# Performance work log

Measured on AMD Instinct MI355X. Metric: run time of the kernel, lower is better.

## Reference

```python
import jax, jax.numpy as jnp
import numpy as np

B, P, D, N, K = 8, 784, 1536, 20000, 9


def setup_inputs() -> dict:
    key = jax.random.key(0)
    k1, k2 = jax.random.split(key)
    x = jax.random.normal(k1, (B, P, D), dtype=jnp.float32)       # patch embeddings [B, P, D]
    memory = jax.random.normal(k2, (N, D), dtype=jnp.float32)     # FAISS memory bank [N, D]
    return {"x": x, "memory": memory, "k": K}


def reference(x, memory, k):
    # Squared L2 distances (FAISS IndexFlatL2 convention): [B, P, N]
    x2 = jnp.sum(x * x, axis=-1, keepdims=True)                   # [B, P, 1]
    m2 = jnp.sum(memory * memory, axis=-1)                        # [N]
    d = x2 + m2[None, None, :] - 2.0 * jnp.einsum('bpd,nd->bpn', x, memory)
    # k nearest (smallest distances, ascending) -> score_patches [B, P, k]
    neg_topk, _ = jax.lax.top_k(-d, k)
    score_patches = -neg_topk
    closest_dist = score_patches[..., 0]                          # [B, P]
    idxmax = jnp.argmax(closest_dist, axis=1)                     # [B]
    # N_b: the k neighbor distances of the worst (max closest-dist) patch
    N_b = jnp.take_along_axis(score_patches, idxmax[:, None, None], axis=1)[:, 0, :]  # [B, k]
    N_b = N_b - jnp.max(N_b, axis=1, keepdims=True)               # numerical stabilization (as in source)
    N_b_exp = jnp.exp(N_b)
    w = 1.0 - jnp.max(N_b_exp, axis=1) / jnp.sum(N_b_exp, axis=1)  # [B]
    score = w * jnp.max(closest_dist, axis=1)                      # [B]
    return score
```

## Files before the change

### kernel.cpp

```cpp
#include <hip/hip_runtime.h>
#include <math.h>

#define B_    8
#define P_    784
#define M_    6272
#define D_    1536
#define N_    20000
#define NC_   4

#define MPAD  6400
#define NPAD2 20224
#define MT2   25
#define NT2   79
#define KT2   24

#define NBLK  625

using bf16x8 = __attribute__((ext_vector_type(8))) __bf16;
using f32x4v = __attribute__((ext_vector_type(4))) float;

#define GLD_LDS16(src, dst)                                            \
  __builtin_amdgcn_global_load_lds(                                    \
      (__attribute__((address_space(1))) const void*)(src),            \
      (__attribute__((address_space(3))) void*)(dst), 16, 0, 0)

__device__ __forceinline__ unsigned short f2bf(float f) {
  union { float f; unsigned u; } v; v.f = f;
  unsigned r = v.u + 0x7fffu + ((v.u >> 16) & 1u);
  return (unsigned short)(r >> 16);
}

__device__ __forceinline__ unsigned fenc(float f) {
  unsigned u = __float_as_uint(f);
  return (u >> 31) ? ~u : (u | 0x80000000u);
}
__device__ __forceinline__ float fdec(unsigned k) {
  return (k >> 31) ? __uint_as_float(k & 0x7FFFFFFFu) : __uint_as_float(~k);
}

__device__ __forceinline__ void convert_one(const float* __restrict__ src,
                                            unsigned short* __restrict__ dst,
                                            float* __restrict__ sq,
                                            int row, int realrows) {
  const int t = threadIdx.x;
  if (row >= realrows) {
    ushort4* w4 = (ushort4*)(dst + (size_t)row * D_);
    for (int i = t; i < D_ / 4; i += 256) w4[i] = ushort4{0, 0, 0, 0};
    if (t == 0) sq[row] = 1e30f;
    return;
  }
  const float4* r4 = (const float4*)(src + (size_t)row * D_);
  ushort4* w4 = (ushort4*)(dst + (size_t)row * D_);
  float s = 0.f;
  for (int i = t; i < D_ / 4; i += 256) {
    float4 v = r4[i];
    s += v.x * v.x + v.y * v.y + v.z * v.z + v.w * v.w;
    w4[i] = ushort4{f2bf(v.x), f2bf(v.y), f2bf(v.z), f2bf(v.w)};
  }
#pragma unroll
  for (int m = 32; m >= 1; m >>= 1) s += __shfl_xor(s, m);
  __shared__ float ws4[4];
  if ((t & 63) == 0) ws4[t >> 6] = s;
  __syncthreads();
  if (t == 0) sq[row] = ws4[0] + ws4[1] + ws4[2] + ws4[3];
}

__global__ void convert_all(const float* __restrict__ x, const float* __restrict__ mem,
                            unsigned short* __restrict__ xbf, unsigned short* __restrict__ mbf,
                            float* __restrict__ x2, float* __restrict__ m2) {
  const int blk = blockIdx.x;
  if (blk < NPAD2) convert_one(mem, mbf, m2, blk, N_);
  else convert_one(x, xbf, x2, blk - NPAD2, M_);
}

__global__ __launch_bounds__(512, 2) void gemm_min8(
    const unsigned short* __restrict__ xbf, const unsigned short* __restrict__ mbf,
    const float* __restrict__ m2, unsigned* __restrict__ closest_enc) {
  __shared__ __attribute__((aligned(16))) char ldsFlat[131072];
  __shared__ float ldsMin[4][256];

  const int NWG = MT2 * NT2;
  const int bid = blockIdx.x;
  const int q = NWG >> 3, r = NWG & 7;
  const int xcd = bid & 7, loc = bid >> 3;
  const int wg = (xcd < r ? xcd * (q + 1) : r * (q + 1) + (xcd - r) * q) + loc;
  const int s = wg / (5 * NT2);
  const int r2 = wg - s * (5 * NT2);
  const int mT = s * 5 + (r2 % 5);
  const int nT = r2 / 5;

  const int tid = threadIdx.x;
  const int lane = tid & 63, wid = tid >> 6;
  const int wm = wid >> 2, wn = wid & 3;
  const int g = lane >> 4, r16 = lane & 15;
  const int mBase = mT * 256, nBase = nT * 256;

  const int stRow = wid * 8 + (lane >> 3);
  const int stA = mBase + stRow;
  const int stB = nBase + stRow;
  const int cswz8 = ((lane & 7) ^ ((lane >> 3) & 7)) * 8;

  const int cs0 = (g * 16) ^ ((r16 & 7) << 4);
  const int rdA = wm * 16384 + r16 * 128;
  const int rdB = wn * 8192 + r16 * 128;

#define STAGE(matsel, srcp, rowb, bufb, h, ktv) do {                       \
    char* dst_ = ldsFlat + (matsel) * 65536 + (bufb) * 32768 +             \
                 (h) * 16384 + wid * 1024;                                 \
    const unsigned short* s_ =                                             \
        (srcp) + (size_t)((rowb) + (h) * 128) * 1536 + (ktv) * 64 + cswz8; \
    GLD_LDS16(s_, dst_);                                                   \
    GLD_LDS16(s_ + 64 * 1536, dst_ + 8192);                                \
  } while (0)

  f32x4v acc[8][4];
#pragma unroll
  for (int i = 0; i < 8; ++i)
#pragma unroll
    for (int j = 0; j < 4; ++j) acc[i][j] = f32x4v{0.f, 0.f, 0.f, 0.f};

  STAGE(1, mbf, stB, 0, 0, 0);
  STAGE(1, mbf, stB, 0, 1, 0);
  STAGE(0, xbf, stA, 0, 0, 0);
  STAGE(0, xbf, stA, 0, 1, 0);
  STAGE(1, mbf, stB, 1, 0, 1);
  STAGE(1, mbf, stB, 1, 1, 1);
  asm volatile("s_waitcnt vmcnt(4)");
  __builtin_amdgcn_s_barrier();
  __builtin_amdgcn_sched_barrier(0);

#pragma unroll 1
  for (int kt = 0; kt < KT2; ++kt) {
    const int bufc = kt & 1;
    const char* Ab = ldsFlat + bufc * 32768;
    const char* Bb = ldsFlat + 65536 + bufc * 32768;
    const bool stgA = (kt + 1) < KT2;
    const bool stgB = (kt + 2) < KT2;
    bf16x8 b0[4], b1[4], a0[4], a1[4];

#pragma unroll
    for (int nf = 0; nf < 4; ++nf) {
      b0[nf] = *(const bf16x8*)(Bb + rdB + nf * 2048 + cs0);
      b1[nf] = *(const bf16x8*)(Bb + rdB + nf * 2048 + (cs0 ^ 64));
    }
#pragma unroll
    for (int mf = 0; mf < 4; ++mf) {
      a0[mf] = *(const bf16x8*)(Ab + rdA + mf * 2048 + cs0);
      a1[mf] = *(const bf16x8*)(Ab + rdA + mf * 2048 + (cs0 ^ 64));
    }
    if (stgA) {
      STAGE(0, xbf, stA, bufc ^ 1, 0, kt + 1);
      STAGE(0, xbf, stA, bufc ^ 1, 1, kt + 1);
    }
    __builtin_amdgcn_s_barrier();
    asm volatile("s_waitcnt lgkmcnt(0)");
    __builtin_amdgcn_s_setprio(1);
#pragma unroll
    for (int mf = 0; mf < 4; ++mf)
#pragma unroll
      for (int nf = 0; nf < 4; ++nf)
        acc[mf][nf] = __builtin_amdgcn_mfma_f32_16x16x32_bf16(a0[mf], b0[nf], acc[mf][nf], 0, 0, 0);
#pragma unroll
    for (int mf = 0; mf < 4; ++mf)
#pragma unroll
      for (int nf = 0; nf < 4; ++nf)
        acc[mf][nf] = __builtin_amdgcn_mfma_f32_16x16x32_bf16(a1[mf], b1[nf], acc[mf][nf], 0, 0, 0);
    __builtin_amdgcn_s_setprio(0);
    __builtin_amdgcn_s_barrier();

#pragma unroll
    for (int mf = 0; mf < 4; ++mf) {
      a0[mf] = *(const bf16x8*)(Ab + rdA + (mf + 4) * 2048 + cs0);
      a1[mf] = *(const bf16x8*)(Ab + rdA + (mf + 4) * 2048 + (cs0 ^ 64));
    }
    if (stgB) {
      STAGE(1, mbf, stB, bufc, 0, kt + 2);
      STAGE(1, mbf, stB, bufc, 1, kt + 2);
    }
    __builtin_amdgcn_s_barrier();
    asm volatile("s_waitcnt lgkmcnt(0)");
    __builtin_amdgcn_s_setprio(1);
#pragma unroll
    for (int mf = 0; mf < 4; ++mf)
#pragma unroll
      for (int nf = 0; nf < 4; ++nf)
        acc[mf + 4][nf] = __builtin_amdgcn_mfma_f32_16x16x32_bf16(a0[mf], b0[nf], acc[mf + 4][nf], 0, 0, 0);
#pragma unroll
    for (int mf = 0; mf < 4; ++mf)
#pragma unroll
      for (int nf = 0; nf < 4; ++nf)
        acc[mf + 4][nf] = __builtin_amdgcn_mfma_f32_16x16x32_bf16(a1[mf], b1[nf], acc[mf + 4][nf], 0, 0, 0);
    __builtin_amdgcn_s_setprio(0);
    if (kt >= 22) {
      asm volatile("s_waitcnt vmcnt(0)");
    } else {
      asm volatile("s_waitcnt vmcnt(4)");
    }
    __builtin_amdgcn_s_barrier();
    __builtin_amdgcn_sched_barrier(0);
  }
#undef STAGE

  float m2v[4];
#pragma unroll
  for (int nf = 0; nf < 4; ++nf) m2v[nf] = m2[nBase + wn * 64 + nf * 16 + r16];
#pragma unroll
  for (int mf = 0; mf < 8; ++mf) {
    float mn[4];
#pragma unroll
    for (int i = 0; i < 4; ++i) {
      float v = m2v[0] - 2.f * acc[mf][0][i];
      v = fminf(v, m2v[1] - 2.f * acc[mf][1][i]);
      v = fminf(v, m2v[2] - 2.f * acc[mf][2][i]);
      v = fminf(v, m2v[3] - 2.f * acc[mf][3][i]);
      mn[i] = v;
    }
#pragma unroll
    for (int msk = 1; msk < 16; msk <<= 1)
#pragma unroll
      for (int i = 0; i < 4; ++i) mn[i] = fminf(mn[i], __shfl_xor(mn[i], msk));
    if (r16 == 0)
#pragma unroll
      for (int i = 0; i < 4; ++i)
        ldsMin[wn][wm * 128 + mf * 16 + g * 4 + i] = mn[i];
  }
  __syncthreads();
  if (tid < 256) {
    float v = fminf(fminf(ldsMin[0][tid], ldsMin[1][tid]),
                    fminf(ldsMin[2][tid], ldsMin[3][tid]));
    atomicMin(&closest_enc[mBase + tid], fenc(v));
  }
}

__global__ void topcand_kernel(const unsigned* __restrict__ closest_enc,
                               const float* __restrict__ x2,
                               int* __restrict__ cand) {
  const int b = blockIdx.x;
  const int t = threadIdx.x;
  __shared__ float cls[P_];
  for (int p = t; p < P_; p += 256) {
    const int row = b * P_ + p;
    cls[p] = x2[row] + fdec(closest_enc[row]);
  }
  __syncthreads();
  __shared__ float wv[4];
  __shared__ int wi_[4];
  __shared__ int picked[NC_];
  for (int r = 0; r < NC_; ++r) {
    float mv = -3e38f; int mi = 1 << 30;
    for (int p = t; p < P_; p += 256) {
      bool skip = false;
      for (int c = 0; c < r; ++c) skip |= (picked[c] == p);
      float v = cls[p];
      if (!skip && (v > mv || (v == mv && p < mi))) { mv = v; mi = p; }
    }
#pragma unroll
    for (int m = 32; m >= 1; m >>= 1) {
      float ov = __shfl_xor(mv, m); int oi = __shfl_xor(mi, m);
      if (ov > mv || (ov == mv && oi < mi)) { mv = ov; mi = oi; }
    }
    if ((t & 63) == 0) { wv[t >> 6] = mv; wi_[t >> 6] = mi; }
    __syncthreads();
    if (t == 0) {
      float bv = wv[0]; int bi = wi_[0];
      for (int w = 1; w < 4; ++w)
        if (wv[w] > bv || (wv[w] == bv && wi_[w] < bi)) { bv = wv[w]; bi = wi_[w]; }
      picked[r] = bi;
      cand[b * NC_ + r] = bi;
    }
    __syncthreads();
  }
}

__device__ __forceinline__ void ins9(float* t, float v) {
  if (v < t[8]) {
    int p = 8;
    while (p > 0 && t[p - 1] > v) { t[p] = t[p - 1]; --p; }
    t[p] = v;
  }
}

__global__ __launch_bounds__(256) void cand_dist9(
    const float* __restrict__ x, const float* __restrict__ mem,
    const float* __restrict__ x2, const float* __restrict__ m2,
    const int* __restrict__ cand, float* __restrict__ ctop) {
  const int wid = threadIdx.x >> 6, lane = threadIdx.x & 63;
  const int blk = blockIdx.x;
  __shared__ float ldsD[32][36];

  for (int batch = 0; batch < 2; ++batch) {
    const int rbase = blk * 32 + wid * 8 + batch * 4;
    float4 m4[4][6];
    float m2r[4];
#pragma unroll
    for (int k = 0; k < 4; ++k) {
      const float4* mrow = (const float4*)(mem + (size_t)(rbase + k) * D_);
#pragma unroll
      for (int j = 0; j < 6; ++j) m4[k][j] = mrow[j * 64 + lane];
      m2r[k] = m2[rbase + k];
    }
    for (int bc = 0; bc < B_ * NC_; ++bc) {
      const int b = bc >> 2;
      const int p = cand[bc];
      const float4* xp = (const float4*)(x + ((size_t)b * P_ + p) * D_);
      float s0 = 0.f, s1 = 0.f, s2 = 0.f, s3 = 0.f;
#pragma unroll
      for (int j = 0; j < 6; ++j) {
        float4 a = xp[j * 64 + lane];
        s0 += a.x * m4[0][j].x + a.y * m4[0][j].y + a.z * m4[0][j].z + a.w * m4[0][j].w;
        s1 += a.x * m4[1][j].x + a.y * m4[1][j].y + a.z * m4[1][j].z + a.w * m4[1][j].w;
        s2 += a.x * m4[2][j].x + a.y * m4[2][j].y + a.z * m4[2][j].z + a.w * m4[2][j].w;
        s3 += a.x * m4[3][j].x + a.y * m4[3][j].y + a.z * m4[3][j].z + a.w * m4[3][j].w;
      }
#pragma unroll
      for (int msk = 32; msk >= 1; msk >>= 1) {
        s0 += __shfl_xor(s0, msk); s1 += __shfl_xor(s1, msk);
        s2 += __shfl_xor(s2, msk); s3 += __shfl_xor(s3, msk);
      }
      if (lane == 0) {
        const float xx = x2[b * P_ + p];
        const int rloc = wid * 8 + batch * 4;
        ldsD[bc][rloc + 0] = xx + m2r[0] - 2.f * s0;
        ldsD[bc][rloc + 1] = xx + m2r[1] - 2.f * s1;
        ldsD[bc][rloc + 2] = xx + m2r[2] - 2.f * s2;
        ldsD[bc][rloc + 3] = xx + m2r[3] - 2.f * s3;
      }
    }
  }
  __syncthreads();
  if (lane < 8) {
    const int bc = wid * 8 + lane;
    float t[9];
#pragma unroll
    for (int i = 0; i < 9; ++i) t[i] = 3e38f;
    for (int i = 0; i < 32; ++i) ins9(t, ldsD[bc][i]);
    float* o = ctop + ((size_t)bc * NBLK + blk) * 9;
#pragma unroll
    for (int i = 0; i < 9; ++i) o[i] = t[i];
  }
}

__global__ void merge_top9(const float* __restrict__ ctop, float* __restrict__ top9) {
  const int bc = blockIdx.x;
  const float* d = ctop + (size_t)bc * (NBLK * 9);
  float t[9];
#pragma unroll
  for (int i = 0; i < 9; ++i) t[i] = 3e38f;
  for (int n = threadIdx.x; n < NBLK * 9; n += 256) ins9(t, d[n]);
  __shared__ float l9[256 * 9];
  __shared__ float l9b[32 * 9];
  for (int i = 0; i < 9; ++i) l9[threadIdx.x * 9 + i] = t[i];
  __syncthreads();
  if (threadIdx.x < 32) {
    float u[9];
#pragma unroll
    for (int i = 0; i < 9; ++i) u[i] = 3e38f;
    for (int s = 0; s < 8; ++s)
      for (int i = 0; i < 9; ++i) ins9(u, l9[(threadIdx.x * 8 + s) * 9 + i]);
    for (int i = 0; i < 9; ++i) l9b[threadIdx.x * 9 + i] = u[i];
  }
  __syncthreads();
  if (threadIdx.x == 0) {
    float u[9];
#pragma unroll
    for (int i = 0; i < 9; ++i) u[i] = 3e38f;
    for (int s = 0; s < 32; ++s)
      for (int i = 0; i < 9; ++i) ins9(u, l9b[s * 9 + i]);
    for (int i = 0; i < 9; ++i) top9[bc * 9 + i] = u[i];
  }
}

__global__ void score_kernel(const float* __restrict__ top9, const int* __restrict__ cand,
                             float* __restrict__ out) {
  const int b = threadIdx.x;
  if (b >= B_) return;
  float bestv = -3e38f; int bestc = 0, bestp = 1 << 30;
  for (int c = 0; c < NC_; ++c) {
    float v = top9[(b * NC_ + c) * 9 + 0];
    int p = cand[b * NC_ + c];
    if (v > bestv || (v == bestv && p < bestp)) { bestv = v; bestc = c; bestp = p; }
  }
  const float* v9 = &top9[(b * NC_ + bestc) * 9];
  float mx = v9[8];
  float sum = 0.f, mxe = 0.f;
  for (int i = 0; i < 9; ++i) {
    float e = expf(v9[i] - mx);
    sum += e;
    if (e > mxe) mxe = e;
  }
  out[b] = (1.f - mxe / sum) * bestv;
}

extern "C" void kernel_launch(void* const* d_in, const int* in_sizes, int n_in,
                              void* d_out, int out_size, void* d_ws, size_t ws_size,
                              hipStream_t stream) {
  const float* x = (const float*)d_in[0];
  const float* mem = (const float*)d_in[1];
  float* out = (float*)d_out;
  char* ws = (char*)d_ws;

  unsigned short* xbf  = (unsigned short*)(ws);
  unsigned short* mbf  = (unsigned short*)(ws + 19660800);
  float* x2            = (float*)(ws + 81788928);
  float* m2            = (float*)(ws + 81814528);
  unsigned* closest_enc= (unsigned*)(ws + 81895424);
  int*   cand          = (int*)  (ws + 81921024);
  float* ctop          = (float*)(ws + 81921152);
  float* top9          = (float*)(ws + 82641152);

  hipMemsetAsync(closest_enc, 0xFF, MPAD * 4, stream);
  convert_all<<<NPAD2 + MPAD, 256, 0, stream>>>(x, mem, xbf, mbf, x2, m2);
  gemm_min8<<<MT2 * NT2, 512, 0, stream>>>(xbf, mbf, m2, closest_enc);
  topcand_kernel<<<B_, 256, 0, stream>>>(closest_enc, x2, cand);
  cand_dist9<<<NBLK, 256, 0, stream>>>(x, mem, x2, m2, cand, ctop);
  merge_top9<<<B_ * NC_, 256, 0, stream>>>(ctop, top9);
  score_kernel<<<1, 64, 0, stream>>>(top9, cand, out);
}
```

Baseline: 551.5 us.

## Switch candidate-screening GEMM from bf16 to fp8 e4m3 scaled MFMA

Quantizes x and memory to fp8 e4m3 instead of bf16 and uses the 16x16x128 f8f6f4 scaled MFMA, halving the K iterations and the bytes staged through LDS. This targets the screening GEMM's MFMA throughput and memory traffic, and also halves the conversion output size. Because fp8 is much less precise, the number of exact-recheck candidates per batch doubles from 4 to 8, which roughly doubles the fp32 rescoring work in cand_dist9 and merge. If the fp8 error still lets the true worst patch fall outside the candidate set, the result could be wrong.

```diff
diff --git a/kernel.cpp b/kernel.cpp
--- a/kernel.cpp
+++ b/kernel.cpp
@@ -1,4 +1,5 @@
 #include <hip/hip_runtime.h>
+#include <hip/hip_fp8.h>
 #include <math.h>
 
 #define B_    8
@@ -6,17 +7,17 @@
 #define M_    6272
 #define D_    1536
 #define N_    20000
-#define NC_   4
+#define NC_   8
 
 #define MPAD  6400
 #define NPAD2 20224
 #define MT2   25
 #define NT2   79
-#define KT2   24
+#define KT2   12
 
 #define NBLK  625
 
-using bf16x8 = __attribute__((ext_vector_type(8))) __bf16;
+using i32x8  = __attribute__((ext_vector_type(8))) int;
 using f32x4v = __attribute__((ext_vector_type(4))) float;
 
 #define GLD_LDS16(src, dst)                                            \
@@ -24,10 +25,9 @@
       (__attribute__((address_space(1))) const void*)(src),            \
       (__attribute__((address_space(3))) void*)(dst), 16, 0, 0)
 
-__device__ __forceinline__ unsigned short f2bf(float f) {
-  union { float f; unsigned u; } v; v.f = f;
-  unsigned r = v.u + 0x7fffu + ((v.u >> 16) & 1u);
-  return (unsigned short)(r >> 16);
+__device__ __forceinline__ unsigned char f2fp8(float v) {
+  __hip_fp8_e4m3 q(v);
+  return (unsigned char)q.__x;
 }
 
 __device__ __forceinline__ unsigned fenc(float f) {
@@ -39,23 +39,25 @@
 }
 
 __device__ __forceinline__ void convert_one(const float* __restrict__ src,
-                                            unsigned short* __restrict__ dst,
+                                            unsigned char* __restrict__ dst,
                                             float* __restrict__ sq,
                                             int row, int realrows) {
   const int t = threadIdx.x;
   if (row >= realrows) {
-    ushort4* w4 = (ushort4*)(dst + (size_t)row * D_);
-    for (int i = t; i < D_ / 4; i += 256) w4[i] = ushort4{0, 0, 0, 0};
+    unsigned* w = (unsigned*)(dst + (size_t)row * D_);
+    for (int i = t; i < D_ / 4; i += 256) w[i] = 0u;
     if (t == 0) sq[row] = 1e30f;
     return;
   }
   const float4* r4 = (const float4*)(src + (size_t)row * D_);
-  ushort4* w4 = (ushort4*)(dst + (size_t)row * D_);
+  unsigned* w = (unsigned*)(dst + (size_t)row * D_);
   float s = 0.f;
   for (int i = t; i < D_ / 4; i += 256) {
     float4 v = r4[i];
     s += v.x * v.x + v.y * v.y + v.z * v.z + v.w * v.w;
-    w4[i] = ushort4{f2bf(v.x), f2bf(v.y), f2bf(v.z), f2bf(v.w)};
+    unsigned pk = (unsigned)f2fp8(v.x) | ((unsigned)f2fp8(v.y) << 8) |
+                  ((unsigned)f2fp8(v.z) << 16) | ((unsigned)f2fp8(v.w) << 24);
+    w[i] = pk;
   }
 #pragma unroll
   for (int m = 32; m >= 1; m >>= 1) s += __shfl_xor(s, m);
@@ -66,15 +68,15 @@
 }
 
 __global__ void convert_all(const float* __restrict__ x, const float* __restrict__ mem,
-                            unsigned short* __restrict__ xbf, unsigned short* __restrict__ mbf,
+                            unsigned char* __restrict__ xq, unsigned char* __restrict__ mq,
                             float* __restrict__ x2, float* __restrict__ m2) {
   const int blk = blockIdx.x;
-  if (blk < NPAD2) convert_one(mem, mbf, m2, blk, N_);
-  else convert_one(x, xbf, x2, blk - NPAD2, M_);
+  if (blk < NPAD2) convert_one(mem, mq, m2, blk, N_);
+  else convert_one(x, xq, x2, blk - NPAD2, M_);
 }
 
 __global__ __launch_bounds__(512, 2) void gemm_min8(
-    const unsigned short* __restrict__ xbf, const unsigned short* __restrict__ mbf,
+    const unsigned char* __restrict__ xq, const unsigned char* __restrict__ mq,
     const float* __restrict__ m2, unsigned* __restrict__ closest_enc) {
   __shared__ __attribute__((aligned(16))) char ldsFlat[131072];
   __shared__ float ldsMin[4][256];
@@ -98,33 +100,42 @@
   const int stRow = wid * 8 + (lane >> 3);
   const int stA = mBase + stRow;
   const int stB = nBase + stRow;
-  const int cswz8 = ((lane & 7) ^ ((lane >> 3) & 7)) * 8;
-
-  const int cs0 = (g * 16) ^ ((r16 & 7) << 4);
+  const int cswz16 = ((lane & 7) ^ ((lane >> 3) & 7)) * 16;
+
+  const int csl = (g * 32) ^ ((r16 & 7) << 4);
+  const int csh = csl ^ 16;
   const int rdA = wm * 16384 + r16 * 128;
   const int rdB = wn * 8192 + r16 * 128;
 
-#define STAGE(matsel, srcp, rowb, bufb, h, ktv) do {                       \
-    char* dst_ = ldsFlat + (matsel) * 65536 + (bufb) * 32768 +             \
-                 (h) * 16384 + wid * 1024;                                 \
-    const unsigned short* s_ =                                             \
-        (srcp) + (size_t)((rowb) + (h) * 128) * 1536 + (ktv) * 64 + cswz8; \
-    GLD_LDS16(s_, dst_);                                                   \
-    GLD_LDS16(s_ + 64 * 1536, dst_ + 8192);                                \
+#define STAGE(matsel, srcp, rowb, bufb, h, ktv) do {                        \
+    char* dst_ = ldsFlat + (matsel) * 65536 + (bufb) * 32768 +              \
+                 (h) * 16384 + wid * 1024;                                  \
+    const unsigned char* s_ =                                               \
+        (srcp) + (size_t)((rowb) + (h) * 128) * 1536 + (ktv) * 128 + cswz16;\
+    GLD_LDS16(s_, dst_);                                                    \
+    GLD_LDS16(s_ + 64 * 1536, dst_ + 8192);                                 \
   } while (0)
 
+#define LDFRAG(base, off) ({                                                \
+    int4 lo_ = *(const int4*)((base) + (off) + csl);                        \
+    int4 hi_ = *(const int4*)((base) + (off) + csh);                        \
+    i32x8{lo_.x, lo_.y, lo_.z, lo_.w, hi_.x, hi_.y, hi_.z, hi_.w}; })
+
+#define MFMA8(a, b, c) __builtin_amdgcn_mfma_scale_f32_16x16x128_f8f6f4(    \
+    (a), (b), (c), 0, 0, 0, 0x7F7F7F7F, 0, 0x7F7F7F7F)
+
   f32x4v acc[8][4];
 #pragma unroll
   for (int i = 0; i < 8; ++i)
 #pragma unroll
     for (int j = 0; j < 4; ++j) acc[i][j] = f32x4v{0.f, 0.f, 0.f, 0.f};
 
-  STAGE(1, mbf, stB, 0, 0, 0);
-  STAGE(1, mbf, stB, 0, 1, 0);
-  STAGE(0, xbf, stA, 0, 0, 0);
-  STAGE(0, xbf, stA, 0, 1, 0);
-  STAGE(1, mbf, stB, 1, 0, 1);
-  STAGE(1, mbf, stB, 1, 1, 1);
+  STAGE(1, mq, stB, 0, 0, 0);
+  STAGE(1, mq, stB, 0, 1, 0);
+  STAGE(0, xq, stA, 0, 0, 0);
+  STAGE(0, xq, stA, 0, 1, 0);
+  STAGE(1, mq, stB, 1, 0, 1);
+  STAGE(1, mq, stB, 1, 1, 1);
   asm volatile("s_waitcnt vmcnt(4)");
   __builtin_amdgcn_s_barrier();
   __builtin_amdgcn_sched_barrier(0);
@@ -136,21 +147,15 @@
     const char* Bb = ldsFlat + 65536 + bufc * 32768;
     const bool stgA = (kt + 1) < KT2;
     const bool stgB = (kt + 2) < KT2;
-    bf16x8 b0[4], b1[4], a0[4], a1[4];
-
-#pragma unroll
-    for (int nf = 0; nf < 4; ++nf) {
-      b0[nf] = *(const bf16x8*)(Bb + rdB + nf * 2048 + cs0);
-      b1[nf] = *(const bf16x8*)(Bb + rdB + nf * 2048 + (cs0 ^ 64));
-    }
-#pragma unroll
-    for (int mf = 0; mf < 4; ++mf) {
-      a0[mf] = *(const bf16x8*)(Ab + rdA + mf * 2048 + cs0);
-      a1[mf] = *(const bf16x8*)(Ab + rdA + mf * 2048 + (cs0 ^ 64));
-    }
+    i32x8 bf[4], af[4];
+
+#pragma unroll
+    for (int nf = 0; nf < 4; ++nf) bf[nf] = LDFRAG(Bb, rdB + nf * 2048);
+#pragma unroll
+    for (int mf = 0; mf < 4; ++mf) af[mf] = LDFRAG(Ab, rdA + mf * 2048);
     if (stgA) {
-      STAGE(0, xbf, stA, bufc ^ 1, 0, kt + 1);
-      STAGE(0, xbf, stA, bufc ^ 1, 1, kt + 1);
+      STAGE(0, xq, stA, bufc ^ 1, 0, kt + 1);
+      STAGE(0, xq, stA, bufc ^ 1, 1, kt + 1);
     }
     __builtin_amdgcn_s_barrier();
     asm volatile("s_waitcnt lgkmcnt(0)");
@@ -159,23 +164,15 @@
     for (int mf = 0; mf < 4; ++mf)
 #pragma unroll
       for (int nf = 0; nf < 4; ++nf)
-        acc[mf][nf] = __builtin_amdgcn_mfma_f32_16x16x32_bf16(a0[mf], b0[nf], acc[mf][nf], 0, 0, 0);
-#pragma unroll
-    for (int mf = 0; mf < 4; ++mf)
-#pragma unroll
-      for (int nf = 0; nf < 4; ++nf)
-        acc[mf][nf] = __builtin_amdgcn_mfma_f32_16x16x32_bf16(a1[mf], b1[nf], acc[mf][nf], 0, 0, 0);
+        acc[mf][nf] = MFMA8(af[mf], bf[nf], acc[mf][nf]);
     __builtin_amdgcn_s_setprio(0);
     __builtin_amdgcn_s_barrier();
 
 #pragma unroll
-    for (int mf = 0; mf < 4; ++mf) {
-      a0[mf] = *(const bf16x8*)(Ab + rdA + (mf + 4) * 2048 + cs0);
-      a1[mf] = *(const bf16x8*)(Ab + rdA + (mf + 4) * 2048 + (cs0 ^ 64));
-    }
+    for (int mf = 0; mf < 4; ++mf) af[mf] = LDFRAG(Ab, rdA + (mf + 4) * 2048);
     if (stgB) {
-      STAGE(1, mbf, stB, bufc, 0, kt + 2);
-      STAGE(1, mbf, stB, bufc, 1, kt + 2);
+      STAGE(1, mq, stB, bufc, 0, kt + 2);
+      STAGE(1, mq, stB, bufc, 1, kt + 2);
     }
     __builtin_amdgcn_s_barrier();
     asm volatile("s_waitcnt lgkmcnt(0)");
@@ -184,14 +181,9 @@
     for (int mf = 0; mf < 4; ++mf)
 #pragma unroll
       for (int nf = 0; nf < 4; ++nf)
-        acc[mf + 4][nf] = __builtin_amdgcn_mfma_f32_16x16x32_bf16(a0[mf], b0[nf], acc[mf + 4][nf], 0, 0, 0);
-#pragma unroll
-    for (int mf = 0; mf < 4; ++mf)
-#pragma unroll
-      for (int nf = 0; nf < 4; ++nf)
-        acc[mf + 4][nf] = __builtin_amdgcn_mfma_f32_16x16x32_bf16(a1[mf], b1[nf], acc[mf + 4][nf], 0, 0, 0);
+        acc[mf + 4][nf] = MFMA8(af[mf], bf[nf], acc[mf + 4][nf]);
     __builtin_amdgcn_s_setprio(0);
-    if (kt >= 22) {
+    if (kt >= KT2 - 2) {
       asm volatile("s_waitcnt vmcnt(0)");
     } else {
       asm volatile("s_waitcnt vmcnt(4)");
@@ -200,6 +192,8 @@
     __builtin_amdgcn_sched_barrier(0);
   }
 #undef STAGE
+#undef LDFRAG
+#undef MFMA8
 
   float m2v[4];
 #pragma unroll
@@ -286,7 +280,7 @@
     const int* __restrict__ cand, float* __restrict__ ctop) {
   const int wid = threadIdx.x >> 6, lane = threadIdx.x & 63;
   const int blk = blockIdx.x;
-  __shared__ float ldsD[32][36];
+  __shared__ float ldsD[B_ * NC_][36];
 
   for (int batch = 0; batch < 2; ++batch) {
     const int rbase = blk * 32 + wid * 8 + batch * 4;
@@ -300,7 +294,7 @@
       m2r[k] = m2[rbase + k];
     }
     for (int bc = 0; bc < B_ * NC_; ++bc) {
-      const int b = bc >> 2;
+      const int b = bc / NC_;
       const int p = cand[bc];
       const float4* xp = (const float4*)(x + ((size_t)b * P_ + p) * D_);
       float s0 = 0.f, s1 = 0.f, s2 = 0.f, s3 = 0.f;
@@ -328,8 +322,8 @@
     }
   }
   __syncthreads();
-  if (lane < 8) {
-    const int bc = wid * 8 + lane;
+  if (lane < 16) {
+    const int bc = wid * 16 + lane;
     float t[9];
 #pragma unroll
     for (int i = 0; i < 9; ++i) t[i] = 3e38f;
@@ -399,18 +393,18 @@
   float* out = (float*)d_out;
   char* ws = (char*)d_ws;
 
-  unsigned short* xbf  = (unsigned short*)(ws);
-  unsigned short* mbf  = (unsigned short*)(ws + 19660800);
-  float* x2            = (float*)(ws + 81788928);
-  float* m2            = (float*)(ws + 81814528);
-  unsigned* closest_enc= (unsigned*)(ws + 81895424);
-  int*   cand          = (int*)  (ws + 81921024);
-  float* ctop          = (float*)(ws + 81921152);
-  float* top9          = (float*)(ws + 82641152);
+  unsigned char* xq    = (unsigned char*)(ws);
+  unsigned char* mq    = (unsigned char*)(ws + 9830400);
+  float* x2            = (float*)(ws + 40894464);
+  float* m2            = (float*)(ws + 40920064);
+  unsigned* closest_enc= (unsigned*)(ws + 41000960);
+  int*   cand          = (int*)  (ws + 41026560);
+  float* ctop          = (float*)(ws + 41026816);
+  float* top9          = (float*)(ws + 42466816);
 
   hipMemsetAsync(closest_enc, 0xFF, MPAD * 4, stream);
-  convert_all<<<NPAD2 + MPAD, 256, 0, stream>>>(x, mem, xbf, mbf, x2, m2);
-  gemm_min8<<<MT2 * NT2, 512, 0, stream>>>(xbf, mbf, m2, closest_enc);
+  convert_all<<<NPAD2 + MPAD, 256, 0, stream>>>(x, mem, xq, mq, x2, m2);
+  gemm_min8<<<MT2 * NT2, 512, 0, stream>>>(xq, mq, m2, closest_enc);
   topcand_kernel<<<B_, 256, 0, stream>>>(closest_enc, x2, cand);
   cand_dist9<<<NBLK, 256, 0, stream>>>(x, mem, x2, m2, cand, ctop);
   merge_top9<<<B_ * NC_, 256, 0, stream>>>(ctop, top9);
```

Measured after the change: 494.5 us. 10.3% less time.
